# Performance work log

Measured on AMD Instinct MI355X. Metric: run time of the kernel, lower is better.

The kernel has to match this reference:

```python
import jax, jax.numpy as jnp
import numpy as np

# fbank band edges (hp.bandmode == 'fbank'), 32 bands over 257 freq bins
EBAND = [0,3,5,8,10,13,15,18,22,25,29,33,38,42,48,53,59,66,73,80,89,97,107,117,128,140,153,167,183,199,216,256]

def _inverse_filter():
    f = np.zeros((len(EBAND), EBAND[-1] + 1), np.float32)
    for i in range(len(EBAND) - 1):
        w = EBAND[i + 1] - EBAND[i]
        for j in range(w):
            f[i, EBAND[i] + j] = 1.0 - j / w
            f[i + 1, EBAND[i] + j] = j / w
    return jnp.asarray(f)  # [32, 257]

def _glin(x, w):
    # GroupedLinear (DeepFilterNet-style, no bias): w [g, in/g, out/g]
    g, gi, go = w.shape
    y = jnp.einsum('...gi,gio->...go', x.reshape(x.shape[:-1] + (g, gi)), w)
    return y.reshape(x.shape[:-1] + (g * go,))

def _prelu(x, a):
    return jnp.where(x >= 0, x, a * x)

def _gru(x, wih, whh, bih, bhh):
    # single-layer torch-style GRU; x [T,B,I], wih/whh [3H, I/H]
    H = whh.shape[-1]
    h0 = jnp.zeros((x.shape[1], H), x.dtype)
    def step(h, xt):
        gi = xt @ wih.T + bih
        gh = h @ whh.T + bhh
        ir, iz, inn = jnp.split(gi, 3, axis=-1)
        hr, hz, hn = jnp.split(gh, 3, axis=-1)
        r = jax.nn.sigmoid(ir + hr)
        z = jax.nn.sigmoid(iz + hz)
        n = jnp.tanh(inn + r * hn)
        hnew = (1.0 - z) * n + z * h
        return hnew, hnew
    _, ys = jax.lax.scan(step, h0, x)
    return ys  # [T,B,H]

def _ggru_layer(x, wih, whh, bih, bhh):
    # grouped GRU layer: weights stacked on leading group axis
    g = wih.shape[0]
    T, B, I = x.shape
    xg = x.reshape(T, B, g, I // g).transpose(2, 0, 1, 3)  # [g,T,B,I/g]
    ys = jax.vmap(_gru)(xg, wih, whh, bih, bhh)            # [g,T,B,H/g]
    return ys.transpose(1, 2, 0, 3).reshape(T, B, -1)

def _shuffle(x, g):
    # channel shuffle between grouped GRU layers
    T, B, H = x.shape
    return x.reshape(T, B, -1, g).swapaxes(2, 3).reshape(T, B, H)

def _forward(main_input, spec, log_power_input, s1_fc_in_w, s1_fc_in_b,
             s1_gru_wih0, s1_gru_whh0, s1_gru_bih0, s1_gru_bhh0,
             s1_gru_wih1, s1_gru_whh1, s1_gru_bih1, s1_gru_bhh1,
             s1_fcout_w, fc_in_low_w, prelu_low, fc_in_high_w, prelu_high,
             gru_low_wih, gru_low_whh, gru_low_bih, gru_low_bhh,
             gru_high_wih, gru_high_whh, gru_high_bih, gru_high_bhh,
             fc_out_low_w, fc_out_high_w, ne, fc):
    B, _, T, F = main_input.shape
    # --- Stage1: pad time, unfold window, keep first ne+1 taps ---
    xp = jnp.pad(main_input, ((0, 0), (0, 0), (ne, ne), (0, 0)))
    win = jnp.stack([xp[:, :, k:k + T] for k in range(ne + 1)], axis=-1)  # [B,1,T,F,ne+1]
    x = win.reshape(B, T, F * (ne + 1))                                   # [B,T,64]
    x0 = (x @ s1_fc_in_w.T + s1_fc_in_b).transpose(1, 0, 2)               # [T,B,32]
    y1 = _gru(x0, s1_gru_wih0, s1_gru_whh0, s1_gru_bih0, s1_gru_bhh0)
    y2 = _gru(y1, s1_gru_wih1, s1_gru_whh1, s1_gru_bih1, s1_gru_bhh1)
    x1 = (y1 + y2).transpose(1, 0, 2)                                     # add_outputs; [B,T,32]
    band_mask = jax.nn.sigmoid(_glin(x1, s1_fcout_w))                     # [B,T,32]
    full_mask = (band_mask @ _inverse_filter()).transpose(0, 2, 1)        # [B,257,T]
    out = spec * full_mask[..., None]                                     # [B,257,T,2]
    # --- low band path ---
    low = jnp.concatenate([log_power_input[:, :, :fc], band_mask], axis=-1)  # [B,T,160]
    low = _prelu(_glin(low, fc_in_low_w), prelu_low).transpose(1, 0, 2)      # [T,B,64]
    acc = jnp.zeros_like(low)
    inp = low
    for l in range(2):  # 2 grouped layers, shuffle between, add_outputs
        inp = _ggru_layer(inp, gru_low_wih[l], gru_low_whh[l], gru_low_bih[l], gru_low_bhh[l])
        if l == 0:
            inp = _shuffle(inp, 2)
        acc = acc + inp
    mask_low = jax.nn.sigmoid(_glin(acc.transpose(1, 0, 2), fc_out_low_w))   # [B,T,128]
    # --- high band path ---
    high = jnp.concatenate([log_power_input[:, :, fc:256], band_mask], axis=-1)  # [B,T,160]
    high = _prelu(_glin(high, fc_in_high_w), prelu_high).transpose(1, 0, 2)      # [T,B,32]
    dfh = _ggru_layer(high, gru_high_wih, gru_high_whh, gru_high_bih, gru_high_bhh)
    mask_high = jax.nn.sigmoid(_glin(dfh.transpose(1, 0, 2), fc_out_high_w))     # [B,T,128]
    # --- fuse masks (rows: 0:fc low, fc:256 high, 256 passthrough) ---
    mask = jnp.concatenate([
        mask_low.transpose(0, 2, 1) * full_mask[:, :fc],
        mask_high.transpose(0, 2, 1) * full_mask[:, fc:256],
        full_mask[:, 256:257],
    ], axis=1)                                                            # [B,257,T]
    spec_out = mask[..., None] * out
    spec_mag = jnp.sqrt(spec_out[..., 0] ** 2 + spec_out[..., 1] ** 2)
    return full_mask, mask, spec_mag, spec_out

def setup_inputs():
    ks = iter(jax.random.split(jax.random.key(0), 48))
    rn = lambda shape, s=1.0: jax.random.normal(next(ks), shape, jnp.float32) * s
    B, T = 256, 256
    return {
        'main_input': rn((B, 1, T, 32)),
        'spec': rn((B, 257, T, 2)),
        'log_power_input': rn((B, T, 256)),
        'n_expand_fbank': 1,
        'freq_cut': 128,
        's1_fc_in_w': rn((32, 64), 0.125),
        's1_fc_in_b': rn((32,), 0.05),
        's1_gru_wih0': rn((96, 32), 0.18),
        's1_gru_whh0': rn((96, 32), 0.18),
        's1_gru_bih0': rn((96,), 0.05),
        's1_gru_bhh0': rn((96,), 0.05),
        's1_gru_wih1': rn((96, 32), 0.18),
        's1_gru_whh1': rn((96, 32), 0.18),
        's1_gru_bih1': rn((96,), 0.05),
        's1_gru_bhh1': rn((96,), 0.05),
        's1_fcout_w': rn((1, 32, 32), 0.18),
        'fc_in_low_w': rn((1, 160, 64), 0.08),
        'prelu_low': jnp.full((1,), 0.25, jnp.float32),
        'fc_in_high_w': rn((2, 80, 16), 0.11),
        'prelu_high': jnp.full((1,), 0.25, jnp.float32),
        'gru_low_wih': rn((2, 2, 96, 32), 0.18),
        'gru_low_whh': rn((2, 2, 96, 32), 0.18),
        'gru_low_bih': rn((2, 2, 96), 0.05),
        'gru_low_bhh': rn((2, 2, 96), 0.05),
        'gru_high_wih': rn((2, 48, 16), 0.25),
        'gru_high_whh': rn((2, 48, 16), 0.25),
        'gru_high_bih': rn((2, 48), 0.05),
        'gru_high_bhh': rn((2, 48), 0.05),
        'fc_out_low_w': rn((1, 64, 128), 0.125),
        'fc_out_high_w': rn((2, 16, 64), 0.25),
    }

def reference(main_input, spec, log_power_input, n_expand_fbank, freq_cut,
              s1_fc_in_w, s1_fc_in_b,
              s1_gru_wih0, s1_gru_whh0, s1_gru_bih0, s1_gru_bhh0,
              s1_gru_wih1, s1_gru_whh1, s1_gru_bih1, s1_gru_bhh1,
              s1_fcout_w, fc_in_low_w, prelu_low, fc_in_high_w, prelu_high,
              gru_low_wih, gru_low_whh, gru_low_bih, gru_low_bhh,
              gru_high_wih, gru_high_whh, gru_high_bih, gru_high_bhh,
              fc_out_low_w, fc_out_high_w):
    return _forward(main_input, spec, log_power_input, s1_fc_in_w, s1_fc_in_b,
                    s1_gru_wih0, s1_gru_whh0, s1_gru_bih0, s1_gru_bhh0,
                    s1_gru_wih1, s1_gru_whh1, s1_gru_bih1, s1_gru_bhh1,
                    s1_fcout_w, fc_in_low_w, prelu_low, fc_in_high_w, prelu_high,
                    gru_low_wih, gru_low_whh, gru_low_bih, gru_low_bhh,
                    gru_high_wih, gru_high_whh, gru_high_bih, gru_high_bhh,
                    fc_out_low_w, fc_out_high_w, int(n_expand_fbank), int(freq_cut))
```

## Files before the change

### kernel.cpp

```cpp
#include <hip/hip_runtime.h>
#include <math.h>

#define Bn 256
#define Tn 256

__constant__ int EB[32] = {0,3,5,8,10,13,15,18,22,25,29,33,38,42,48,53,59,66,73,80,89,97,107,117,128,140,153,167,183,199,216,256};

__device__ __forceinline__ float fsig(float x){ return __builtin_amdgcn_rcpf(1.f + __expf(-x)); }
__device__ __forceinline__ float ftanh(float x){ return 1.f - 2.f*__builtin_amdgcn_rcpf(1.f + __expf(2.f*x)); }

__device__ __forceinline__ void gload16(const float* g, float* l){
  __builtin_amdgcn_global_load_lds((const __attribute__((address_space(1))) void*)g,
                                   (__attribute__((address_space(3))) void*)l, 16, 0, 0);
}

#define KEEP(x) asm volatile("" : "+v"(x))

typedef float v2f __attribute__((ext_vector_type(2)));

#define DOT16(res, X, W) do{ float _s0=0.f,_s1=0.f,_s2=0.f,_s3=0.f; \
  _Pragma("unroll") for (int _e=0;_e<4;++_e){ \
    _s0=fmaf((X)[_e],(W)[_e],_s0); _s1=fmaf((X)[4+_e],(W)[4+_e],_s1); \
    _s2=fmaf((X)[8+_e],(W)[8+_e],_s2); _s3=fmaf((X)[12+_e],(W)[12+_e],_s3);} \
  (res)=(_s0+_s1)+(_s2+_s3); }while(0)

#define DOT8(res, X, W) do{ float _s0=0.f,_s1=0.f; \
  _Pragma("unroll") for (int _e=0;_e<4;++_e){ \
    _s0=fmaf((X)[_e],(W)[_e],_s0); _s1=fmaf((X)[4+_e],(W)[4+_e],_s1);} \
  (res)=_s0+_s1; }while(0)

#define FMA44(A, X, W) do{ \
  (A)[0]=fmaf((X).x,(W)[0].x,(A)[0]); (A)[1]=fmaf((X).x,(W)[0].y,(A)[1]); (A)[2]=fmaf((X).x,(W)[0].z,(A)[2]); (A)[3]=fmaf((X).x,(W)[0].w,(A)[3]); \
  (A)[0]=fmaf((X).y,(W)[1].x,(A)[0]); (A)[1]=fmaf((X).y,(W)[1].y,(A)[1]); (A)[2]=fmaf((X).y,(W)[1].z,(A)[2]); (A)[3]=fmaf((X).y,(W)[1].w,(A)[3]); \
  (A)[0]=fmaf((X).z,(W)[2].x,(A)[0]); (A)[1]=fmaf((X).z,(W)[2].y,(A)[1]); (A)[2]=fmaf((X).z,(W)[2].z,(A)[2]); (A)[3]=fmaf((X).z,(W)[2].w,(A)[3]); \
  (A)[0]=fmaf((X).w,(W)[3].x,(A)[0]); (A)[1]=fmaf((X).w,(W)[3].y,(A)[1]); (A)[2]=fmaf((X).w,(W)[3].z,(A)[2]); (A)[3]=fmaf((X).w,(W)[3].w,(A)[3]); \
}while(0)

__global__ __launch_bounds__(256) void k0(const float* __restrict__ wfc, const float* __restrict__ bfc,
    const float* __restrict__ wih0, const float* __restrict__ bih0,
    const float* __restrict__ glw_ih, const float* __restrict__ glb_ih,
    const float* __restrict__ ghw_ih, const float* __restrict__ ghb_ih,
    float* __restrict__ wcT, float* __restrict__ bc,
    float* __restrict__ wBT, float* __restrict__ bB){
  int i = blockIdx.x*256 + threadIdx.x;
  if (i < 6144){
    int k = i/96, o = i - (i/96)*96;
    float s = 0.f;
    #pragma unroll
    for (int kk = 0; kk < 32; ++kk) s = fmaf(wih0[o*32+kk], wfc[kk*64+k], s);
    wcT[i] = s;
  } else if (i < 6240){
    int o = i - 6144;
    float s = bih0[o];
    #pragma unroll
    for (int kk = 0; kk < 32; ++kk) s = fmaf(wih0[o*32+kk], bfc[kk], s);
    bc[o] = s;
  } else if (i < 13920){
    int j = i - 6240;
    if (j < 6144){
      int og = j >> 7, rem = j & 127, k = rem >> 2, jj = rem & 3;
      int o = og*4 + jj; int g = o/96, r = o - g*96;
      wBT[j] = glw_ih[(g*96 + r)*32 + k];
    } else {
      int j2 = j - 6144;
      int oh = j2 >> 6, rem = j2 & 63, k = rem >> 2, jj = rem & 3;
      int o = oh*4 + jj; int g = o/48, r = o - g*48;
      wBT[j] = ghw_ih[(g*48 + r)*16 + k];
    }
  } else if (i < 14208){
// ... 21 lines not shown
  const int og = tid >> 3, btg = tid & 7;
  if (og >= 24) return;
  float acc[4][4];
  #pragma unroll
  for (int bj = 0; bj < 4; ++bj){ acc[bj][0]=0.f; acc[bj][1]=0.f; acc[bj][2]=0.f; acc[bj][3]=0.f; }
  for (int fq = 0; fq < 8; ++fq){
    float4 wvp[4], wvc[4];
    #pragma unroll
    for (int i = 0; i < 4; ++i){
      int f = fq*4 + i;
      wvp[i] = *(const float4*)&wcT[(2*f)*96 + og*4];
      wvc[i] = *(const float4*)&wcT[(2*f+1)*96 + og*4];
    }
    #pragma unroll
    for (int bj = 0; bj < 4; ++bj){
      int btl = btg + 8*bj;
      float4 xp = *(const float4*)&mbuf[btl*36 + fq*4];
      float4 xc = *(const float4*)&mbuf[(btl+1)*36 + fq*4];
      FMA44(acc[bj], xp, wvp);
      FMA44(acc[bj], xc, wvc);
    }
  }
  float4 bias = *(const float4*)&bc[og*4];
  #pragma unroll
  for (int bj = 0; bj < 4; ++bj){
    int btl = btg + 8*bj;
    float4 o;
    o.x = acc[bj][0] + bias.x; o.y = acc[bj][1] + bias.y;
    o.z = acc[bj][2] + bias.z; o.w = acc[bj][3] + bias.w;
    *(float4*)&gi0[(bt0 + btl)*96 + og*4] = o;
  }
}

__global__ __launch_bounds__(128,1) void kS1(const float* __restrict__ gi0,
    const float* __restrict__ whh0, const float* __restrict__ bhh0,
    const float* __restrict__ wih1, const float* __restrict__ whh1,
    const float* __restrict__ bih1, const float* __restrict__ bhh1,
    const float* __restrict__ fco, float* __restrict__ bmA)
{
  __shared__ __attribute__((aligned(16))) float gib[2][3072];
  __shared__ __attribute__((aligned(16))) float y1buf[2][32];
  __shared__ __attribute__((aligned(16))) float h1arr[32];
  __shared__ __attribute__((aligned(16))) float h2arr[32];
  const int tid = threadIdx.x;
  const int wid = tid >> 6;
  const int lane = tid & 63;
  const int q = lane >> 5, h = lane & 31, ko = q*16;
  const int b = blockIdx.x;
  const float* gsrc = gi0 + b*24576;

  float wI[3][16], wH[3][16], wF[16];
  float b0, b1, b2, b3;
  if (wid == 0){
    #pragma unroll
    for (int g = 0; g < 3; ++g){
      const float* w = whh0 + (g*32+h)*32 + ko;
      #pragma unroll
      for (int k = 0; k < 16; ++k){ wI[g][k] = w[k]; wH[g][k] = w[k]; }
    }
    #pragma unroll
    for (int k = 0; k < 16; ++k) wF[k] = 0.f;
    b0 = bhh0[h]; b1 = bhh0[32+h]; b2 = bhh0[64+h]; b3 = 0.f;
    #pragma unroll
    for (int c0 = 0; c0 < 2; ++c0)
      for (int it = 0; it < 12; ++it)
        gload16(gsrc + c0*3072 + it*256 + lane*4, &gib[c0][it*256]);
    asm volatile("s_waitcnt vmcnt(0)" ::: "memory");
  } else {
    #pragma unroll
    for (int g = 0; g < 3; ++g){
      const float* wi = wih1 + (g*32+h)*32 + ko;
      const float* wh = whh1 + (g*32+h)*32 + ko;
      #pragma unroll
      for (int k = 0; k < 16; ++k){ wI[g][k] = wi[k]; wH[g][k] = wh[k]; }
    }
    #pragma unroll
    for (int k = 0; k < 16; ++k) wF[k] = fco[(ko+k)*32 + h];
    b0 = bih1[h] + bhh1[h];
    b1 = bih1[32+h] + bhh1[32+h];
    b2 = bih1[64+h];
    b3 = bhh1[64+h];
  }
  #pragma unroll
  for (int g = 0; g < 3; ++g){
    #pragma unroll
    for (int k = 0; k < 16; ++k){ KEEP(wI[g][k]); KEEP(wH[g][k]); }
  }
  #pragma unroll
  for (int k = 0; k < 16; ++k) KEEP(wF[k]);
  __syncthreads();

  float hv[16];
  #pragma unroll
  for (int k = 0; k < 16; ++k) hv[k] = 0.f;
  float hOwn = 0.f;
  float c_r = 0.f, c_z = 0.f, c_n = 0.f, p_r = 0.f, p_z = 0.f, p_n = 0.f;

  for (int s = 0; s <= Tn; ++s){
    __syncthreads();
    if (wid == 0){
      if (s < Tn){
        const int t = s;
        if ((t & 31) == 0){
          if (t){
            int c = t >> 5;
            if (c < 7){
              for (int it = 0; it < 12; ++it)
                gload16(gsrc + (c+1)*3072 + it*256 + lane*4, &gib[(c+1)&1][it*256]);
            }
          }
          const float* gt = &gib[(t>>5)&1][(t&31)*96];
          c_r = gt[h]; c_z = gt[32+h]; c_n = gt[64+h];
        } else { c_r = p_r; c_z = p_z; c_n = p_n; }
        if ((t+1) & 31){
          const float* gn = &gib[((t+1)>>5)&1][((t+1)&31)*96];
          p_r = gn[h]; p_z = gn[32+h]; p_n = gn[64+h];
        }
        float pr, pz, pn;
        DOT16(pr, hv, wI[0]); DOT16(pz, hv, wI[1]); DOT16(pn, hv, wI[2]);
        pr += __shfl_xor(pr,32); pz += __shfl_xor(pz,32); pn += __shfl_xor(pn,32);
        float r = fsig(c_r + pr + b0);
        float z = fsig(c_z + pz + b1);
        float nn = ftanh(c_n + r*(pn + b2));
        float hn = nn + z*(hOwn - nn);
        hOwn = hn;
        h1arr[h] = hn;
        if (q == 0) y1buf[s & 1][h] = hn;
        *(float4*)&hv[0]  = *(const float4*)&h1arr[ko+0];
        *(float4*)&hv[4]  = *(const float4*)&h1arr[ko+4];
        *(float4*)&hv[8]  = *(const float4*)&h1arr[ko+8];
        *(float4*)&hv[12] = *(const float4*)&h1arr[ko+12];
      }
    } else {
      if (s >= 1){
        const int t = s - 1;
        const float* yb = y1buf[t & 1];
        float xv[16];
        *(float4*)&xv[0]  = *(const float4*)&yb[ko+0];
        *(float4*)&xv[4]  = *(const float4*)&yb[ko+4];
        *(float4*)&xv[8]  = *(const float4*)&yb[ko+8];
        *(float4*)&xv[12] = *(const float4*)&yb[ko+12];
        float ur, uz, ui, vr, vz, vh;
        DOT16(ur, xv, wI[0]); DOT16(uz, xv, wI[1]); DOT16(ui, xv, wI[2]);
        DOT16(vr, hv, wH[0]); DOT16(vz, hv, wH[1]); DOT16(vh, hv, wH[2]);
        float qr = ur + vr, qz = uz + vz;
        qr += __shfl_xor(qr,32); qz += __shfl_xor(qz,32);
        ui += __shfl_xor(ui,32); vh += __shfl_xor(vh,32);
        float r1 = fsig(qr + b0);
        float z1 = fsig(qz + b1);
        float n1 = ftanh(ui + b2 + r1*(vh + b3));
        float hn = n1 + z1*(hOwn - n1);
        hOwn = hn;
        h2arr[h] = hn;
        *(float4*)&hv[0]  = *(const float4*)&h2arr[ko+0];
        *(float4*)&hv[4]  = *(const float4*)&h2arr[ko+4];
        *(float4*)&hv[8]  = *(const float4*)&h2arr[ko+8];
        *(float4*)&hv[12] = *(const float4*)&h2arr[ko+12];
        float sf = 0.f;
        #pragma unroll
        for (int k = 0; k < 16; ++k) sf = fmaf(xv[k] + hv[k], wF[k], sf);
        sf += __shfl_xor(sf,32);
        if (q == 0) bmA[(b*Tn + t)*32 + h] = fsig(sf);
      }
    }
  }
}

__global__ __launch_bounds__(256) void kP(const float* __restrict__ lpi,
    const float* __restrict__ bmA,
    const float* __restrict__ wlo, const float* __restrict__ plo,
    const float* __restrict__ whi, const float* __restrict__ phi,
    const float* __restrict__ wBT, const float* __restrict__ bB,
    float* __restrict__ giL, float* __restrict__ giH)
{
  __shared__ float xb[32*292];
  __shared__ float mb[32*100];
  const int tid = threadIdx.x;
  const int b = blockIdx.x >> 3;
  const int t0 = (blockIdx.x & 7)*32;
  const int bt0 = b*256 + t0;
  #pragma unroll
  for (int j = 0; j < 8; ++j){
    int idx = j*256 + tid;
    int row = idx >> 6, c4 = idx & 63;
    float4 v = *(const float4*)&lpi[(bt0 + row)*256 + c4*4];
    *(float4*)&xb[row*292 + c4*4] = v;
  }
  {
    int row = tid >> 3, c4 = tid & 7;
    float4 v = *(const float4*)&bmA[(bt0 + row)*32 + c4*4];
    *(float4*)&xb[row*292 + 256 + c4*4] = v;
  }
  __syncthreads();
  const int og = tid >> 3, btg = tid & 7;
  if (og < 16){
    float acc[4][4];
    #pragma unroll
    for (int bj = 0; bj < 4; ++bj){ acc[bj][0]=0.f; acc[bj][1]=0.f; acc[bj][2]=0.f; acc[bj][3]=0.f; }
    for (int kq = 0; kq < 40; ++kq){
      int k0_ = kq*4;
      int kk = (k0_ < 128) ? k0_ : k0_ + 128;
      float4 wv[4];
      #pragma unroll
      for (int i = 0; i < 4; ++i) wv[i] = *(const float4*)&wlo[(k0_+i)*64 + og*4];
      #pragma unroll
      for (int bj = 0; bj < 4; ++bj){
        float4 xv = *(const float4*)&xb[(btg + 8*bj)*292 + kk];
        FMA44(acc[bj], xv, wv);
      }
    }
    const float a = plo[0];
    #pragma unroll
    for (int bj = 0; bj < 4; ++bj){
      float4 m;
      m.x = acc[bj][0] >= 0.f ? acc[bj][0] : a*acc[bj][0];
      m.y = acc[bj][1] >= 0.f ? acc[bj][1] : a*acc[bj][1];
      m.z = acc[bj][2] >= 0.f ? acc[bj][2] : a*acc[bj][2];
      m.w = acc[bj][3] >= 0.f ? acc[bj][3] : a*acc[bj][3];
      *(float4*)&mb[(btg + 8*bj)*100 + og*4] = m;
    }
  } else if (og < 24){
    int o0 = (og - 16)*4;
    int g = o0 >> 4, r0 = o0 & 15;
    int xoff = 128 + g*80;
    float acc[4][4];
    #pragma unroll
    for (int bj = 0; bj < 4; ++bj){ acc[bj][0]=0.f; acc[bj][1]=0.f; acc[bj][2]=0.f; acc[bj][3]=0.f; }
    for (int kq = 0; kq < 20; ++kq){
      int k0_ = kq*4;
      float4 wv[4];
      #pragma unroll
      for (int i = 0; i < 4; ++i) wv[i] = *(const float4*)&whi[(g*80 + k0_ + i)*16 + r0];
      #pragma unroll
      for (int bj = 0; bj < 4; ++bj){
        float4 xv = *(const float4*)&xb[(btg + 8*bj)*292 + xoff + k0_];
        FMA44(acc[bj], xv, wv);
      }
    }
    const float a = phi[0];
    #pragma unroll
    for (int bj = 0; bj < 4; ++bj){
      float4 m;
      m.x = acc[bj][0] >= 0.f ? acc[bj][0] : a*acc[bj][0];
      m.y = acc[bj][1] >= 0.f ? acc[bj][1] : a*acc[bj][1];
      m.z = acc[bj][2] >= 0.f ? acc[bj][2] : a*acc[bj][2];
      m.w = acc[bj][3] >= 0.f ? acc[bj][3] : a*acc[bj][3];
      *(float4*)&mb[(btg + 8*bj)*100 + 64 + o0] = m;
    }
  }
  __syncthreads();
  for (int og2 = og; og2 < 72; og2 += 32){
    int woff, kbase, K, obase, dstride;
    float* dst;
    float4 bias;
    if (og2 < 48){
      woff = og2*128; kbase = (og2 >= 24) ? 32 : 0; K = 32;
      obase = og2*4; dst = giL; dstride = 192;
      bias = *(const float4*)&bB[obase];
    } else {
      int oh = og2 - 48;
      woff = 6144 + oh*64;
      int o0 = oh*4; int g = o0/48;
      kbase = 64 + g*16; K = 16;
      obase = o0; dst = giH; dstride = 96;
      bias = *(const float4*)&bB[192 + o0];
    }
    float acc[4][4];
    #pragma unroll
    for (int bj = 0; bj < 4; ++bj){ acc[bj][0]=0.f; acc[bj][1]=0.f; acc[bj][2]=0.f; acc[bj][3]=0.f; }
// ... 195 lines not shown
            asm volatile("s_waitcnt vmcnt(6)" ::: "memory");
          } else {
            asm volatile("s_waitcnt vmcnt(0)" ::: "memory");
          }
        }
        const float* gt = &gib[((t>>4)&1)*1536 + (t&15)*96 + g*48];
        c_r = gt[h]; c_z = gt[16+h]; c_n = gt[32+h];
      } else { c_r = p_r; c_z = p_z; c_n = p_n; }
      if ((t+1) & 15){
        const float* gn = &gib[(((t+1)>>4)&1)*1536 + ((t+1)&15)*96 + g*48];
        p_r = gn[h]; p_z = gn[16+h]; p_n = gn[32+h];
      }
      float pr, pz, pn;
      DOT8(pr, hv, ah[0]); DOT8(pz, hv, ah[1]); DOT8(pn, hv, ah[2]);
      pr += __shfl_xor(pr,16); pz += __shfl_xor(pz,16); pn += __shfl_xor(pn,16);
      float r = fsig(c_r + pr + bhr);
      float z = fsig(c_z + pz + bhz);
      float nn = ftanh(c_n + r*(pn + bhn));
      float hn = nn + z*(hOwn - nn);
      hOwn = hn;
      harr[g*16 + h] = hn;
      *(float4*)&hv[0] = *(const float4*)&harr[g*16 + ko + 0];
      *(float4*)&hv[4] = *(const float4*)&harr[g*16 + ko + 4];
      if (qh == 0) dfh[(b*256 + t)*32 + g*16 + h] = hn;
    }
  }
}

__global__ __launch_bounds__(256) void k7(const float* __restrict__ acc,
    const float* __restrict__ dfh, const float* __restrict__ bmA,
    const float* __restrict__ wlo, const float* __restrict__ whi,
    const float* __restrict__ spec, float* __restrict__ out)
{
  __shared__ float accs[32][65];
  __shared__ float dfhs[32][33];
  __shared__ float bmt[32][33];
  __shared__ float frcs[257];
  __shared__ int   ibds[257];
  const int tid = threadIdx.x;
  const int b  = blockIdx.x >> 3;
  const int t0 = (blockIdx.x & 7) * 32;
  for (int idx = tid; idx < 32*16; idx += 256){
    int tl = idx >> 4, c4 = (idx & 15)*4;
    float4 v = *(const float4*)&acc[(b*256 + t0 + tl)*64 + c4];
    accs[tl][c4] = v.x; accs[tl][c4+1] = v.y; accs[tl][c4+2] = v.z; accs[tl][c4+3] = v.w;
  }
  for (int idx = tid; idx < 32*8; idx += 256){
    int tl = idx >> 3, c4 = (idx & 7)*4;
    float4 v = *(const float4*)&dfh[(b*256 + t0 + tl)*32 + c4];
    dfhs[tl][c4] = v.x; dfhs[tl][c4+1] = v.y; dfhs[tl][c4+2] = v.z; dfhs[tl][c4+3] = v.w;
    float4 u = *(const float4*)&bmA[(b*Tn + t0 + tl)*32 + c4];
    bmt[tl][c4] = u.x; bmt[tl][c4+1] = u.y; bmt[tl][c4+2] = u.z; bmt[tl][c4+3] = u.w;
  }
  for (int f = tid; f < 257; f += 256){
    int i = 0;
    #pragma unroll
    for (int k = 1; k < 31; ++k) if (f >= EB[k]) i = k;
    ibds[f] = i;
    frcs[f] = (f < 256) ? (float)(f - EB[i]) / (float)(EB[i+1] - EB[i]) : 0.f;
  }
  __syncthreads();
  const int tl = tid & 31, fo = tid >> 5;
  float* out1 = out + 16842752;
  float* out2 = out + 2*16842752;
  float* out3 = out + 3*16842752;
  const float2* sp2 = (const float2*)spec;
  {
    float p[16];
    #pragma unroll
    for (int j = 0; j < 16; ++j) p[j] = 0.f;
    for (int i = 0; i < 64; ++i){
      float a = accs[tl][i];
      const float4* wr = (const float4*)&wlo[i*128 + fo*16];
      #pragma unroll
      for (int j4 = 0; j4 < 4; ++j4){
        float4 wv = wr[j4];
        p[j4*4+0] = fmaf(a, wv.x, p[j4*4+0]);
        p[j4*4+1] = fmaf(a, wv.y, p[j4*4+1]);
        p[j4*4+2] = fmaf(a, wv.z, p[j4*4+2]);
        p[j4*4+3] = fmaf(a, wv.w, p[j4*4+3]);
      }
    }
    #pragma unroll
    for (int j = 0; j < 16; ++j){
      int f = fo*16 + j;
      int i = ibds[f]; float fr = frcs[f];
      float full = bmt[tl][i]*(1.f - fr) + bmt[tl][i+1]*fr;
      float m = fsig(p[j])*full;
      int base = (b*257 + f)*Tn + t0 + tl;
      float2 s = sp2[base];
      float fm = full*m;
      float sx = s.x*fm, sy = s.y*fm;
      out[base]  = full;
      out1[base] = m;
      out2[base] = sqrtf(sx*sx + sy*sy);
      *(v2f*)&out3[base*2] = (v2f){sx, sy};
    }
  }
  {
    float p[16];
    #pragma unroll
    for (int j = 0; j < 16; ++j) p[j] = 0.f;
    const int g = fo >> 2, ob = (fo & 3)*16;
    for (int i = 0; i < 16; ++i){
      float a = dfhs[tl][g*16 + i];
      const float4* wr = (const float4*)&whi[(g*16 + i)*64 + ob];
      #pragma unroll
      for (int j4 = 0; j4 < 4; ++j4){
        float4 wv = wr[j4];
        p[j4*4+0] = fmaf(a, wv.x, p[j4*4+0]);
        p[j4*4+1] = fmaf(a, wv.y, p[j4*4+1]);
        p[j4*4+2] = fmaf(a, wv.z, p[j4*4+2]);
        p[j4*4+3] = fmaf(a, wv.w, p[j4*4+3]);
      }
    }
    #pragma unroll
    for (int j = 0; j < 16; ++j){
      int f = 128 + fo*16 + j;
      int i = ibds[f]; float fr = frcs[f];
      float full = bmt[tl][i]*(1.f - fr) + bmt[tl][i+1]*fr;
      float m = fsig(p[j])*full;
      int base = (b*257 + f)*Tn + t0 + tl;
      float2 s = sp2[base];
      float fm = full*m;
      float sx = s.x*fm, sy = s.y*fm;
      out[base]  = full;
      out1[base] = m;
      out2[base] = sqrtf(sx*sx + sy*sy);
      *(v2f*)&out3[base*2] = (v2f){sx, sy};
    }
  }
  if (fo == 0){
    int base = (b*257 + 256)*Tn + t0 + tl;
    out[base]  = 0.f;
    out1[base] = 0.f;
    out2[base] = 0.f;
    *(v2f*)&out3[base*2] = (v2f){0.f, 0.f};
  }
}

extern "C" void kernel_launch(void* const* d_in, const int* in_sizes, int n_in,
                              void* d_out, int out_size, void* d_ws, size_t ws_size,
                              hipStream_t stream){
  const float* mi   = (const float*)d_in[0];
  const float* spec = (const float*)d_in[1];
  const float* lpi  = (const float*)d_in[2];
  const float* s1w  = (const float*)d_in[5];
  const float* s1b  = (const float*)d_in[6];
  const float* wih0 = (const float*)d_in[7];
  const float* whh0 = (const float*)d_in[8];
  const float* bih0 = (const float*)d_in[9];
  const float* bhh0 = (const float*)d_in[10];
  const float* wih1 = (const float*)d_in[11];
  const float* whh1 = (const float*)d_in[12];
  const float* bih1 = (const float*)d_in[13];
  const float* bhh1 = (const float*)d_in[14];
  const float* fco  = (const float*)d_in[15];
  const float* filw = (const float*)d_in[16];
  const float* plo  = (const float*)d_in[17];
  const float* fihw = (const float*)d_in[18];
  const float* phi  = (const float*)d_in[19];
  const float* glw_ih = (const float*)d_in[20];
  const float* glw_hh = (const float*)d_in[21];
  const float* glb_ih = (const float*)d_in[22];
  const float* glb_hh = (const float*)d_in[23];
  const float* ghw_ih = (const float*)d_in[24];
  const float* ghw_hh = (const float*)d_in[25];
  const float* ghb_ih = (const float*)d_in[26];
  const float* ghb_hh = (const float*)d_in[27];
  const float* folw = (const float*)d_in[28];
  const float* fohw = (const float*)d_in[29];

  float* outf = (float*)d_out;
  float* giL  = outf;
  float* gi0  = outf + 12582912;
  float* giH  = outf + 18874368;

  float* ws  = (float*)d_ws;
  float* wcT = ws;
  float* bc  = ws + 6144;
  float* wBT = ws + 6240;
  float* bB  = ws + 13920;
  float* bmA = ws + 14336;
  float* acc = ws + 2111488;
  float* dfh = ws + 6305792;
  float* out = (float*)d_out;

  k0<<<56, 256, 0, stream>>>(s1w, s1b, wih0, bih0, glw_ih, glb_ih, ghw_ih, ghb_ih,
                             wcT, bc, wBT, bB);
  k1<<<2048, 256, 0, stream>>>(mi, wcT, bc, gi0);
  kS1<<<256, 128, 0, stream>>>(gi0, whh0, bhh0, wih1, whh1, bih1, bhh1, fco, bmA);
  kP<<<2048, 256, 0, stream>>>(lpi, bmA, filw, plo, fihw, phi, wBT, bB, giL, giH);
  kR2<<<320, 256, 0, stream>>>(giL, giH, glw_ih, glw_hh, glb_ih, glb_hh,
                               ghw_hh, ghb_hh, acc, dfh);
  k7<<<2048, 256, 0, stream>>>(acc, dfh, bmA, folw, fohw, spec, out);
}
```

Before: 584.0 us.

## Overlap stage-1 GRU with log-power projection and vectorize output kernel

New measurement: 483.3 us. 17.2% less time.

```diff
diff --git a/kernel.cpp b/kernel.cpp
--- a/kernel.cpp
+++ b/kernel.cpp
@@ -15,8 +15,6 @@
 }
 
 #define KEEP(x) asm volatile("" : "+v"(x))
-
-typedef float v2f __attribute__((ext_vector_type(2)));
 
 #define DOT16(res, X, W) do{ float _s0=0.f,_s1=0.f,_s2=0.f,_s3=0.f; \
   _Pragma("unroll") for (int _e=0;_e<4;++_e){ \
@@ -35,6 +33,9 @@
   (A)[0]=fmaf((X).z,(W)[2].x,(A)[0]); (A)[1]=fmaf((X).z,(W)[2].y,(A)[1]); (A)[2]=fmaf((X).z,(W)[2].z,(A)[2]); (A)[3]=fmaf((X).z,(W)[2].w,(A)[3]); \
   (A)[0]=fmaf((X).w,(W)[3].x,(A)[0]); (A)[1]=fmaf((X).w,(W)[3].y,(A)[1]); (A)[2]=fmaf((X).w,(W)[3].z,(A)[2]); (A)[3]=fmaf((X).w,(W)[3].w,(A)[3]); \
 }while(0)
+
+#define FMA4V(P, AV, S) do{ (P).x=fmaf((AV).x,(S),(P).x); (P).y=fmaf((AV).y,(S),(P).y); \
+  (P).z=fmaf((AV).z,(S),(P).z); (P).w=fmaf((AV).w,(S),(P).w); }while(0)
 
 __global__ __launch_bounds__(256) void k0(const float* __restrict__ wfc, const float* __restrict__ bfc,
     const float* __restrict__ wih0, const float* __restrict__ bih0,
@@ -122,180 +123,240 @@
   }
 }
 
-__global__ __launch_bounds__(128,1) void kS1(const float* __restrict__ gi0,
+__global__ __launch_bounds__(128,1) void kSP(const float* __restrict__ gi0,
     const float* __restrict__ whh0, const float* __restrict__ bhh0,
     const float* __restrict__ wih1, const float* __restrict__ whh1,
     const float* __restrict__ bih1, const float* __restrict__ bhh1,
-    const float* __restrict__ fco, float* __restrict__ bmA)
+    const float* __restrict__ fco, float* __restrict__ bmA,
+    const float* __restrict__ lpi,
+    const float* __restrict__ wlo, const float* __restrict__ whi,
+    float* __restrict__ pmid)
 {
-  __shared__ __attribute__((aligned(16))) float gib[2][3072];
-  __shared__ __attribute__((aligned(16))) float y1buf[2][32];
-  __shared__ __attribute__((aligned(16))) float h1arr[32];
-  __shared__ __attribute__((aligned(16))) float h2arr[32];
+  __shared__ __attribute__((aligned(16))) float smem[8320];
   const int tid = threadIdx.x;
-  const int wid = tid >> 6;
-  const int lane = tid & 63;
-  const int q = lane >> 5, h = lane & 31, ko = q*16;
-  const int b = blockIdx.x;
-  const float* gsrc = gi0 + b*24576;
-
-  float wI[3][16], wH[3][16], wF[16];
-  float b0, b1, b2, b3;
-  if (wid == 0){
+  if (blockIdx.x < 256){
+    float* gib   = smem;
+    float* y1buf = smem + 6144;
+    float* h1arr = smem + 6208;
+    float* h2arr = smem + 6240;
+    const int wid = tid >> 6;
+    const int lane = tid & 63;
+    const int q = lane >> 5, h = lane & 31, ko = q*16;
+    const int b = blockIdx.x;
+    const float* gsrc = gi0 + b*24576;
+
+    float wI[3][16], wH[3][16], wF[16];
+    float b0, b1, b2, b3;
+    if (wid == 0){
+      #pragma unroll
+      for (int g = 0; g < 3; ++g){
+        const float* w = whh0 + (g*32+h)*32 + ko;
+        #pragma unroll
+        for (int k = 0; k < 16; ++k){ wI[g][k] = w[k]; wH[g][k] = w[k]; }
+      }
+      #pragma unroll
+      for (int k = 0; k < 16; ++k) wF[k] = 0.f;
+      b0 = bhh0[h]; b1 = bhh0[32+h]; b2 = bhh0[64+h]; b3 = 0.f;
+      #pragma unroll
+      for (int c0 = 0; c0 < 2; ++c0)
+        for (int it = 0; it < 12; ++it)
+          gload16(gsrc + c0*3072 + it*256 + lane*4, &gib[c0*3072 + it*256]);
+      asm volatile("s_waitcnt vmcnt(0)" ::: "memory");
+    } else {
+      #pragma unroll
+      for (int g = 0; g < 3; ++g){
+        const float* wi = wih1 + (g*32+h)*32 + ko;
+        const float* wh = whh1 + (g*32+h)*32 + ko;
+        #pragma unroll
+        for (int k = 0; k < 16; ++k){ wI[g][k] = wi[k]; wH[g][k] = wh[k]; }
+      }
+      #pragma unroll
+      for (int k = 0; k < 16; ++k) wF[k] = fco[(ko+k)*32 + h];
+      b0 = bih1[h] + bhh1[h];
+      b1 = bih1[32+h] + bhh1[32+h];
+      b2 = bih1[64+h];
+      b3 = bhh1[64+h];
+    }
     #pragma unroll
     for (int g = 0; g < 3; ++g){
-      const float* w = whh0 + (g*32+h)*32 + ko;
-      #pragma unroll
-      for (int k = 0; k < 16; ++k){ wI[g][k] = w[k]; wH[g][k] = w[k]; }
-    }
-    #pragma unroll
-    for (int k = 0; k < 16; ++k) wF[k] = 0.f;
-    b0 = bhh0[h]; b1 = bhh0[32+h]; b2 = bhh0[64+h]; b3 = 0.f;
-    #pragma unroll
-    for (int c0 = 0; c0 < 2; ++c0)
-      for (int it = 0; it < 12; ++it)
-        gload16(gsrc + c0*3072 + it*256 + lane*4, &gib[c0][it*256]);
-    asm volatile("s_waitcnt vmcnt(0)" ::: "memory");
+      #pragma unroll
+      for (int k = 0; k < 16; ++k){ KEEP(wI[g][k]); KEEP(wH[g][k]); }
+    }
+    #pragma unroll
+    for (int k = 0; k < 16; ++k) KEEP(wF[k]);
+    __syncthreads();
+
+    float hv[16];
+    #pragma unroll
+    for (int k = 0; k < 16; ++k) hv[k] = 0.f;
+    float hOwn = 0.f;
+    float c_r = 0.f, c_z = 0.f, c_n = 0.f, p_r = 0.f, p_z = 0.f, p_n = 0.f;
+
+    for (int s = 0; s <= Tn; ++s){
+      __syncthreads();
+      if (wid == 0){
+        if (s < Tn){
+          const int t = s;
+          if ((t & 31) == 0){
+            if (t){
+              int c = t >> 5;
+              if (c < 7){
+                for (int it = 0; it < 12; ++it)
+                  gload16(gsrc + (c+1)*3072 + it*256 + lane*4, &gib[((c+1)&1)*3072 + it*256]);
+              }
+            }
+            const float* gt = &gib[((t>>5)&1)*3072 + (t&31)*96];
+            c_r = gt[h]; c_z = gt[32+h]; c_n = gt[64+h];
+          } else { c_r = p_r; c_z = p_z; c_n = p_n; }
+          if ((t+1) & 31){
+            const float* gn = &gib[(((t+1)>>5)&1)*3072 + ((t+1)&31)*96];
+            p_r = gn[h]; p_z = gn[32+h]; p_n = gn[64+h];
+          }
+          float pr, pz, pn;
+          DOT16(pr, hv, wI[0]); DOT16(pz, hv, wI[1]); DOT16(pn, hv, wI[2]);
+          pr += __shfl_xor(pr,32); pz += __shfl_xor(pz,32); pn += __shfl_xor(pn,32);
+          float r = fsig(c_r + pr + b0);
+          float z = fsig(c_z + pz + b1);
+          float nn = ftanh(c_n + r*(pn + b2));
+          float hn = nn + z*(hOwn - nn);
+          hOwn = hn;
+          h1arr[h] = hn;
+          if (q == 0) y1buf[(s & 1)*32 + h] = hn;
+          *(float4*)&hv[0]  = *(const float4*)&h1arr[ko+0];
+          *(float4*)&hv[4]  = *(const float4*)&h1arr[ko+4];
+          *(float4*)&hv[8]  = *(const float4*)&h1arr[ko+8];
+          *(float4*)&hv[12] = *(const float4*)&h1arr[ko+12];
+        }
+      } else {
+        if (s >= 1){
+          const int t = s - 1;
+          const float* yb = &y1buf[(t & 1)*32];
+          float xv[16];
+          *(float4*)&xv[0]  = *(const float4*)&yb[ko+0];
+          *(float4*)&xv[4]  = *(const float4*)&yb[ko+4];
+          *(float4*)&xv[8]  = *(const float4*)&yb[ko+8];
+          *(float4*)&xv[12] = *(const float4*)&yb[ko+12];
+          float ur, uz, ui, vr, vz, vh;
+          DOT16(ur, xv, wI[0]); DOT16(uz, xv, wI[1]); DOT16(ui, xv, wI[2]);
+          DOT16(vr, hv, wH[0]); DOT16(vz, hv, wH[1]); DOT16(vh, hv, wH[2]);
+          float qr = ur + vr, qz = uz + vz;
+          qr += __shfl_xor(qr,32); qz += __shfl_xor(qz,32);
+          ui += __shfl_xor(ui,32); vh += __shfl_xor(vh,32);
+          float r1 = fsig(qr + b0);
+          float z1 = fsig(qz + b1);
+          float n1 = ftanh(ui + b2 + r1*(vh + b3));
+          float hn = n1 + z1*(hOwn - n1);
+          hOwn = hn;
+          h2arr[h] = hn;
+          *(float4*)&hv[0]  = *(const float4*)&h2arr[ko+0];
+          *(float4*)&hv[4]  = *(const float4*)&h2arr[ko+4];
+          *(float4*)&hv[8]  = *(const float4*)&h2arr[ko+8];
+          *(float4*)&hv[12] = *(const float4*)&h2arr[ko+12];
+          float sf = 0.f;
+          #pragma unroll
+          for (int k = 0; k < 16; ++k) sf = fmaf(xv[k] + hv[k], wF[k], sf);
+          sf += __shfl_xor(sf,32);
+          if (q == 0) bmA[(b*Tn + t)*32 + h] = fsig(sf);
+        }
+      }
+    }
   } else {
-    #pragma unroll
-    for (int g = 0; g < 3; ++g){
-      const float* wi = wih1 + (g*32+h)*32 + ko;
-      const float* wh = whh1 + (g*32+h)*32 + ko;
-      #pragma unroll
-      for (int k = 0; k < 16; ++k){ wI[g][k] = wi[k]; wH[g][k] = wh[k]; }
-    }
-    #pragma unroll
-    for (int k = 0; k < 16; ++k) wF[k] = fco[(ko+k)*32 + h];
-    b0 = bih1[h] + bhh1[h];
-    b1 = bih1[32+h] + bhh1[32+h];
-    b2 = bih1[64+h];
-    b3 = bhh1[64+h];
-  }
-  #pragma unroll
-  for (int g = 0; g < 3; ++g){
-    #pragma unroll
-    for (int k = 0; k < 16; ++k){ KEEP(wI[g][k]); KEEP(wH[g][k]); }
-  }
-  #pragma unroll
-  for (int k = 0; k < 16; ++k) KEEP(wF[k]);
-  __syncthreads();
-
-  float hv[16];
-  #pragma unroll
-  for (int k = 0; k < 16; ++k) hv[k] = 0.f;
-  float hOwn = 0.f;
-  float c_r = 0.f, c_z = 0.f, c_n = 0.f, p_r = 0.f, p_z = 0.f, p_n = 0.f;
-
-  for (int s = 0; s <= Tn; ++s){
+    float* xb = smem;
+    const int blk = blockIdx.x - 256;
+    const int b = blk >> 3;
+    const int t0 = (blk & 7)*32;
+    const int bt0 = b*256 + t0;
+    #pragma unroll
+    for (int j = 0; j < 16; ++j){
+      int idx = j*128 + tid;
+      int row = idx >> 6, c4 = idx & 63;
+      float4 v = *(const float4*)&lpi[(bt0 + row)*256 + c4*4];
+      *(float4*)&xb[row*260 + c4*4] = v;
+    }
     __syncthreads();
-    if (wid == 0){
-      if (s < Tn){
-        const int t = s;
-        if ((t & 31) == 0){
-          if (t){
-            int c = t >> 5;
-            if (c < 7){
-              for (int it = 0; it < 12; ++it)
-                gload16(gsrc + (c+1)*3072 + it*256 + lane*4, &gib[(c+1)&1][it*256]);
-            }
+    const int og = tid >> 3, btg = tid & 7;
+    for (int og2 = og; og2 < 24; og2 += 16){
+      float acc[4][4];
+      #pragma unroll
+      for (int bj = 0; bj < 4; ++bj){ acc[bj][0]=0.f; acc[bj][1]=0.f; acc[bj][2]=0.f; acc[bj][3]=0.f; }
+      int obase;
+      if (og2 < 16){
+        for (int kq = 0; kq < 32; ++kq){
+          int k0_ = kq*4;
+          float4 wv[4];
+          #pragma unroll
+          for (int i = 0; i < 4; ++i) wv[i] = *(const float4*)&wlo[(k0_+i)*64 + og2*4];
+          #pragma unroll
+          for (int bj = 0; bj < 4; ++bj){
+            float4 xv = *(const float4*)&xb[(btg + 8*bj)*260 + k0_];
+            FMA44(acc[bj], xv, wv);
           }
-          const float* gt = &gib[(t>>5)&1][(t&31)*96];
-          c_r = gt[h]; c_z = gt[32+h]; c_n = gt[64+h];
-        } else { c_r = p_r; c_z = p_z; c_n = p_n; }
-        if ((t+1) & 31){
-          const float* gn = &gib[((t+1)>>5)&1][((t+1)&31)*96];
-          p_r = gn[h]; p_z = gn[32+h]; p_n = gn[64+h];
         }
-        float pr, pz, pn;
-        DOT16(pr, hv, wI[0]); DOT16(pz, hv, wI[1]); DOT16(pn, hv, wI[2]);
-        pr += __shfl_xor(pr,32); pz += __shfl_xor(pz,32); pn += __shfl_xor(pn,32);
-        float r = fsig(c_r + pr + b0);
-        float z = fsig(c_z + pz + b1);
-        float nn = ftanh(c_n + r*(pn + b2));
-        float hn = nn + z*(hOwn - nn);
-        hOwn = hn;
-        h1arr[h] = hn;
-        if (q == 0) y1buf[s & 1][h] = hn;
-        *(float4*)&hv[0]  = *(const float4*)&h1arr[ko+0];
-        *(float4*)&hv[4]  = *(const float4*)&h1arr[ko+4];
-        *(float4*)&hv[8]  = *(const float4*)&h1arr[ko+8];
-        *(float4*)&hv[12] = *(const float4*)&h1arr[ko+12];
-      }
-    } else {
-      if (s >= 1){
-        const int t = s - 1;
-        const float* yb = y1buf[t & 1];
-        float xv[16];
-        *(float4*)&xv[0]  = *(const float4*)&yb[ko+0];
-        *(float4*)&xv[4]  = *(const float4*)&yb[ko+4];
-        *(float4*)&xv[8]  = *(const float4*)&yb[ko+8];
-        *(float4*)&xv[12] = *(const float4*)&yb[ko+12];
-        float ur, uz, ui, vr, vz, vh;
-        DOT16(ur, xv, wI[0]); DOT16(uz, xv, wI[1]); DOT16(ui, xv, wI[2]);
-        DOT16(vr, hv, wH[0]); DOT16(vz, hv, wH[1]); DOT16(vh, hv, wH[2]);
-        float qr = ur + vr, qz = uz + vz;
-        qr += __shfl_xor(qr,32); qz += __shfl_xor(qz,32);
-        ui += __shfl_xor(ui,32); vh += __shfl_xor(vh,32);
-        float r1 = fsig(qr + b0);
-        float z1 = fsig(qz + b1);
-        float n1 = ftanh(ui + b2 + r1*(vh + b3));
-        float hn = n1 + z1*(hOwn - n1);
-        hOwn = hn;
-        h2arr[h] = hn;
-        *(float4*)&hv[0]  = *(const float4*)&h2arr[ko+0];
-        *(float4*)&hv[4]  = *(const float4*)&h2arr[ko+4];
-        *(float4*)&hv[8]  = *(const float4*)&h2arr[ko+8];
-        *(float4*)&hv[12] = *(const float4*)&h2arr[ko+12];
-        float sf = 0.f;
-        #pragma unroll
-        for (int k = 0; k < 16; ++k) sf = fmaf(xv[k] + hv[k], wF[k], sf);
-        sf += __shfl_xor(sf,32);
-        if (q == 0) bmA[(b*Tn + t)*32 + h] = fsig(sf);
+        obase = og2*4;
+      } else {
+        int o0 = (og2 - 16)*4;
+        int g = o0 >> 4, r0 = o0 & 15;
+        int xoff = 128 + g*80;
+        int nk = (g == 0) ? 20 : 12;
+        for (int kq = 0; kq < nk; ++kq){
+          int k0_ = kq*4;
+          float4 wv[4];
+          #pragma unroll
+          for (int i = 0; i < 4; ++i) wv[i] = *(const float4*)&whi[(g*80 + k0_ + i)*16 + r0];
+          #pragma unroll
+          for (int bj = 0; bj < 4; ++bj){
+            float4 xv = *(const float4*)&xb[(btg + 8*bj)*260 + xoff + k0_];
+            FMA44(acc[bj], xv, wv);
+          }
+        }
+        obase = 64 + o0;
+      }
+      #pragma unroll
+      for (int bj = 0; bj < 4; ++bj){
+        int btl = btg + 8*bj;
+        float4 o;
+        o.x = acc[bj][0]; o.y = acc[bj][1]; o.z = acc[bj][2]; o.w = acc[bj][3];
+        *(float4*)&pmid[(bt0 + btl)*96 + obase] = o;
       }
     }
   }
 }
 
-__global__ __launch_bounds__(256) void kP(const float* __restrict__ lpi,
-    const float* __restrict__ bmA,
+__global__ __launch_bounds__(256) void kPb(const float* __restrict__ bmA,
+    const float* __restrict__ pmid,
     const float* __restrict__ wlo, const float* __restrict__ plo,
     const float* __restrict__ whi, const float* __restrict__ phi,
     const float* __restrict__ wBT, const float* __restrict__ bB,
     float* __restrict__ giL, float* __restrict__ giH)
 {
-  __shared__ float xb[32*292];
+  __shared__ float bmb[32*36];
   __shared__ float mb[32*100];
   const int tid = threadIdx.x;
   const int b = blockIdx.x >> 3;
   const int t0 = (blockIdx.x & 7)*32;
   const int bt0 = b*256 + t0;
-  #pragma unroll
-  for (int j = 0; j < 8; ++j){
-    int idx = j*256 + tid;
-    int row = idx >> 6, c4 = idx & 63;
-    float4 v = *(const float4*)&lpi[(bt0 + row)*256 + c4*4];
-    *(float4*)&xb[row*292 + c4*4] = v;
-  }
   {
     int row = tid >> 3, c4 = tid & 7;
     float4 v = *(const float4*)&bmA[(bt0 + row)*32 + c4*4];
-    *(float4*)&xb[row*292 + 256 + c4*4] = v;
+    *(float4*)&bmb[row*36 + c4*4] = v;
   }
   __syncthreads();
   const int og = tid >> 3, btg = tid & 7;
   if (og < 16){
     float acc[4][4];
     #pragma unroll
-    for (int bj = 0; bj < 4; ++bj){ acc[bj][0]=0.f; acc[bj][1]=0.f; acc[bj][2]=0.f; acc[bj][3]=0.f; }
-    for (int kq = 0; kq < 40; ++kq){
+    for (int bj = 0; bj < 4; ++bj){
+      float4 p = *(const float4*)&pmid[(bt0 + btg + 8*bj)*96 + og*4];
+      acc[bj][0] = p.x; acc[bj][1] = p.y; acc[bj][2] = p.z; acc[bj][3] = p.w;
+    }
+    for (int kq = 0; kq < 8; ++kq){
       int k0_ = kq*4;
-      int kk = (k0_ < 128) ? k0_ : k0_ + 128;
       float4 wv[4];
       #pragma unroll
-      for (int i = 0; i < 4; ++i) wv[i] = *(const float4*)&wlo[(k0_+i)*64 + og*4];
+      for (int i = 0; i < 4; ++i) wv[i] = *(const float4*)&wlo[(128 + k0_ + i)*64 + og*4];
       #pragma unroll
       for (int bj = 0; bj < 4; ++bj){
-        float4 xv = *(const float4*)&xb[(btg + 8*bj)*292 + kk];
+        float4 xv = *(const float4*)&bmb[(btg + 8*bj)*36 + k0_];
         FMA44(acc[bj], xv, wv);
       }
     }
@@ -312,19 +373,23 @@
   } else if (og < 24){
     int o0 = (og - 16)*4;
     int g = o0 >> 4, r0 = o0 & 15;
-    int xoff = 128 + g*80;
     float acc[4][4];
     #pragma unroll
-    for (int bj = 0; bj < 4; ++bj){ acc[bj][0]=0.f; acc[bj][1]=0.f; acc[bj][2]=0.f; acc[bj][3]=0.f; }
-    for (int kq = 0; kq < 20; ++kq){
-      int k0_ = kq*4;
-      float4 wv[4];
-      #pragma unroll
-      for (int i = 0; i < 4; ++i) wv[i] = *(const float4*)&whi[(g*80 + k0_ + i)*16 + r0];
-      #pragma unroll
-      for (int bj = 0; bj < 4; ++bj){
-        float4 xv = *(const float4*)&xb[(btg + 8*bj)*292 + xoff + k0_];
-        FMA44(acc[bj], xv, wv);
+    for (int bj = 0; bj < 4; ++bj){
+      float4 p = *(const float4*)&pmid[(bt0 + btg + 8*bj)*96 + 64 + o0];
+      acc[bj][0] = p.x; acc[bj][1] = p.y; acc[bj][2] = p.z; acc[bj][3] = p.w;
+    }
+    if (g == 1){
+      for (int kq = 0; kq < 8; ++kq){
+        int k0_ = 48 + kq*4;
+        float4 wv[4];
+        #pragma unroll
+        for (int i = 0; i < 4; ++i) wv[i] = *(const float4*)&whi[(80 + k0_ + i)*16 + r0];
+        #pragma unroll
+        for (int bj = 0; bj < 4; ++bj){
+          float4 xv = *(const float4*)&bmb[(btg + 8*bj)*36 + kq*4];
+          FMA44(acc[bj], xv, wv);
+        }
       }
     }
     const float a = phi[0];
@@ -586,25 +651,28 @@
     const float* __restrict__ wlo, const float* __restrict__ whi,
     const float* __restrict__ spec, float* __restrict__ out)
 {
-  __shared__ float accs[32][65];
-  __shared__ float dfhs[32][33];
-  __shared__ float bmt[32][33];
+  __shared__ float accsT[64*36];
+  __shared__ float dfhsT[32*36];
+  __shared__ float bmtT[32*36];
   __shared__ float frcs[257];
   __shared__ int   ibds[257];
   const int tid = threadIdx.x;
   const int b  = blockIdx.x >> 3;
   const int t0 = (blockIdx.x & 7) * 32;
-  for (int idx = tid; idx < 32*16; idx += 256){
+  for (int idx = tid; idx < 512; idx += 256){
     int tl = idx >> 4, c4 = (idx & 15)*4;
     float4 v = *(const float4*)&acc[(b*256 + t0 + tl)*64 + c4];
-    accs[tl][c4] = v.x; accs[tl][c4+1] = v.y; accs[tl][c4+2] = v.z; accs[tl][c4+3] = v.w;
-  }
-  for (int idx = tid; idx < 32*8; idx += 256){
-    int tl = idx >> 3, c4 = (idx & 7)*4;
+    accsT[(c4+0)*36 + tl] = v.x; accsT[(c4+1)*36 + tl] = v.y;
+    accsT[(c4+2)*36 + tl] = v.z; accsT[(c4+3)*36 + tl] = v.w;
+  }
+  {
+    int tl = tid >> 3, c4 = (tid & 7)*4;
     float4 v = *(const float4*)&dfh[(b*256 + t0 + tl)*32 + c4];
-    dfhs[tl][c4] = v.x; dfhs[tl][c4+1] = v.y; dfhs[tl][c4+2] = v.z; dfhs[tl][c4+3] = v.w;
+    dfhsT[(c4+0)*36 + tl] = v.x; dfhsT[(c4+1)*36 + tl] = v.y;
+    dfhsT[(c4+2)*36 + tl] = v.z; dfhsT[(c4+3)*36 + tl] = v.w;
     float4 u = *(const float4*)&bmA[(b*Tn + t0 + tl)*32 + c4];
-    bmt[tl][c4] = u.x; bmt[tl][c4+1] = u.y; bmt[tl][c4+2] = u.z; bmt[tl][c4+3] = u.w;
+    bmtT[(c4+0)*36 + tl] = u.x; bmtT[(c4+1)*36 + tl] = u.y;
+    bmtT[(c4+2)*36 + tl] = u.z; bmtT[(c4+3)*36 + tl] = u.w;
   }
   for (int f = tid; f < 257; f += 256){
     int i = 0;
@@ -614,82 +682,101 @@
     frcs[f] = (f < 256) ? (float)(f - EB[i]) / (float)(EB[i+1] - EB[i]) : 0.f;
   }
   __syncthreads();
-  const int tl = tid & 31, fo = tid >> 5;
+  const int fq = tid >> 3, tq = tid & 7;
   float* out1 = out + 16842752;
   float* out2 = out + 2*16842752;
   float* out3 = out + 3*16842752;
-  const float2* sp2 = (const float2*)spec;
+
   {
-    float p[16];
-    #pragma unroll
-    for (int j = 0; j < 16; ++j) p[j] = 0.f;
+    float4 p[4];
+    #pragma unroll
+    for (int jf = 0; jf < 4; ++jf) p[jf] = make_float4(0.f,0.f,0.f,0.f);
     for (int i = 0; i < 64; ++i){
-      float a = accs[tl][i];
-      const float4* wr = (const float4*)&wlo[i*128 + fo*16];
-      #pragma unroll
-      for (int j4 = 0; j4 < 4; ++j4){
-        float4 wv = wr[j4];
-        p[j4*4+0] = fmaf(a, wv.x, p[j4*4+0]);
-        p[j4*4+1] = fmaf(a, wv.y, p[j4*4+1]);
-        p[j4*4+2] = fmaf(a, wv.z, p[j4*4+2]);
-        p[j4*4+3] = fmaf(a, wv.w, p[j4*4+3]);
-      }
-    }
-    #pragma unroll
-    for (int j = 0; j < 16; ++j){
-      int f = fo*16 + j;
+      float4 av = *(const float4*)&accsT[i*36 + tq*4];
+      float4 wv = *(const float4*)&wlo[i*128 + fq*4];
+      FMA4V(p[0], av, wv.x); FMA4V(p[1], av, wv.y);
+      FMA4V(p[2], av, wv.z); FMA4V(p[3], av, wv.w);
+    }
+    #pragma unroll
+    for (int jf = 0; jf < 4; ++jf){
+      int f = fq*4 + jf;
       int i = ibds[f]; float fr = frcs[f];
-      float full = bmt[tl][i]*(1.f - fr) + bmt[tl][i+1]*fr;
-      float m = fsig(p[j])*full;
-      int base = (b*257 + f)*Tn + t0 + tl;
-      float2 s = sp2[base];
-      float fm = full*m;
-      float sx = s.x*fm, sy = s.y*fm;
-      out[base]  = full;
-      out1[base] = m;
-      out2[base] = sqrtf(sx*sx + sy*sy);
-      *(v2f*)&out3[base*2] = (v2f){sx, sy};
+      float4 b0v = *(const float4*)&bmtT[i*36 + tq*4];
+      float4 b1v = *(const float4*)&bmtT[(i+1)*36 + tq*4];
+      float4 full;
+      full.x = b0v.x*(1.f-fr) + b1v.x*fr; full.y = b0v.y*(1.f-fr) + b1v.y*fr;
+      full.z = b0v.z*(1.f-fr) + b1v.z*fr; full.w = b0v.w*(1.f-fr) + b1v.w*fr;
+      float4 m;
+      m.x = fsig(p[jf].x)*full.x; m.y = fsig(p[jf].y)*full.y;
+      m.z = fsig(p[jf].z)*full.z; m.w = fsig(p[jf].w)*full.w;
+      int base = (b*257 + f)*Tn + t0 + tq*4;
+      float4 s01 = *(const float4*)&spec[base*2];
+      float4 s23 = *(const float4*)&spec[base*2 + 4];
+      float fm0 = full.x*m.x, fm1 = full.y*m.y, fm2 = full.z*m.z, fm3 = full.w*m.w;
+      float sx0 = s01.x*fm0, sy0 = s01.y*fm0;
+      float sx1 = s01.z*fm1, sy1 = s01.w*fm1;
+      float sx2 = s23.x*fm2, sy2 = s23.y*fm2;
+      float sx3 = s23.z*fm3, sy3 = s23.w*fm3;
+      *(float4*)&out[base]  = full;
+      *(float4*)&out1[base] = m;
+      float4 mag;
+      mag.x = sqrtf(sx0*sx0 + sy0*sy0); mag.y = sqrtf(sx1*sx1 + sy1*sy1);
+      mag.z = sqrtf(sx2*sx2 + sy2*sy2); mag.w = sqrtf(sx3*sx3 + sy3*sy3);
+      *(float4*)&out2[base] = mag;
+      *(float4*)&out3[base*2]     = make_float4(sx0, sy0, sx1, sy1);
+      *(float4*)&out3[base*2 + 4] = make_float4(sx2, sy2, sx3, sy3);
     }
   }
   {
-    float p[16];
-    #pragma unroll
-    for (int j = 0; j < 16; ++j) p[j] = 0.f;
-    const int g = fo >> 2, ob = (fo & 3)*16;
+    const int g = fq >> 4;
+    const int col = (fq & 15)*4;
+    float4 p[4];
+    #pragma unroll
+    for (int jf = 0; jf < 4; ++jf) p[jf] = make_float4(0.f,0.f,0.f,0.f);
     for (int i = 0; i < 16; ++i){
-      float a = dfhs[tl][g*16 + i];
-      const float4* wr = (const float4*)&whi[(g*16 + i)*64 + ob];
-      #pragma unroll
-      for (int j4 = 0; j4 < 4; ++j4){
-        float4 wv = wr[j4];
-        p[j4*4+0] = fmaf(a, wv.x, p[j4*4+0]);
-        p[j4*4+1] = fmaf(a, wv.y, p[j4*4+1]);
-        p[j4*4+2] = fmaf(a, wv.z, p[j4*4+2]);
-        p[j4*4+3] = fmaf(a, wv.w, p[j4*4+3]);
-      }
-    }
-    #pragma unroll
-    for (int j = 0; j < 16; ++j){
-      int f = 128 + fo*16 + j;
+      float4 dv = *(const float4*)&dfhsT[(g*16 + i)*36 + tq*4];
+      float4 wv = *(const float4*)&whi[(g*16 + i)*64 + col];
+      FMA4V(p[0], dv, wv.x); FMA4V(p[1], dv, wv.y);
+      FMA4V(p[2], dv, wv.z); FMA4V(p[3], dv, wv.w);
+    }
+    #pragma unroll
+    for (int jf = 0; jf < 4; ++jf){
+      int f = 128 + fq*4 + jf;
       int i = ibds[f]; float fr = frcs[f];
-      float full = bmt[tl][i]*(1.f - fr) + bmt[tl][i+1]*fr;
-      float m = fsig(p[j])*full;
-      int base = (b*257 + f)*Tn + t0 + tl;
-      float2 s = sp2[base];
-      float fm = full*m;
-      float sx = s.x*fm, sy = s.y*fm;
-      out[base]  = full;
-      out1[base] = m;
-      out2[base] = sqrtf(sx*sx + sy*sy);
-      *(v2f*)&out3[base*2] = (v2f){sx, sy};
-    }
-  }
-  if (fo == 0){
-    int base = (b*257 + 256)*Tn + t0 + tl;
-    out[base]  = 0.f;
-    out1[base] = 0.f;
-    out2[base] = 0.f;
-    *(v2f*)&out3[base*2] = (v2f){0.f, 0.f};
+      float4 b0v = *(const float4*)&bmtT[i*36 + tq*4];
+      float4 b1v = *(const float4*)&bmtT[(i+1)*36 + tq*4];
+      float4 full;
+      full.x = b0v.x*(1.f-fr) + b1v.x*fr; full.y = b0v.y*(1.f-fr) + b1v.y*fr;
+      full.z = b0v.z*(1.f-fr) + b1v.z*fr; full.w = b0v.w*(1.f-fr) + b1v.w*fr;
+      float4 m;
+      m.x = fsig(p[jf].x)*full.x; m.y = fsig(p[jf].y)*full.y;
+      m.z = fsig(p[jf].z)*full.z; m.w = fsig(p[jf].w)*full.w;
+      int base = (b*257 + f)*Tn + t0 + tq*4;
+      float4 s01 = *(const float4*)&spec[base*2];
+      float4 s23 = *(const float4*)&spec[base*2 + 4];
+      float fm0 = full.x*m.x, fm1 = full.y*m.y, fm2 = full.z*m.z, fm3 = full.w*m.w;
+      float sx0 = s01.x*fm0, sy0 = s01.y*fm0;
+      float sx1 = s01.z*fm1, sy1 = s01.w*fm1;
+      float sx2 = s23.x*fm2, sy2 = s23.y*fm2;
+      float sx3 = s23.z*fm3, sy3 = s23.w*fm3;
+      *(float4*)&out[base]  = full;
+      *(float4*)&out1[base] = m;
+      float4 mag;
+      mag.x = sqrtf(sx0*sx0 + sy0*sy0); mag.y = sqrtf(sx1*sx1 + sy1*sy1);
+      mag.z = sqrtf(sx2*sx2 + sy2*sy2); mag.w = sqrtf(sx3*sx3 + sy3*sy3);
+      *(float4*)&out2[base] = mag;
+      *(float4*)&out3[base*2]     = make_float4(sx0, sy0, sx1, sy1);
+      *(float4*)&out3[base*2 + 4] = make_float4(sx2, sy2, sx3, sy3);
+    }
+  }
+  if (tid < 8){
+    int base = (b*257 + 256)*Tn + t0 + tid*4;
+    float4 z = make_float4(0.f,0.f,0.f,0.f);
+    *(float4*)&out[base]  = z;
+    *(float4*)&out1[base] = z;
+    *(float4*)&out2[base] = z;
+    *(float4*)&out3[base*2]     = z;
+    *(float4*)&out3[base*2 + 4] = z;
   }
 }
 
@@ -730,21 +817,23 @@
   float* gi0  = outf + 12582912;
   float* giH  = outf + 18874368;
 
-  float* ws  = (float*)d_ws;
-  float* wcT = ws;
-  float* bc  = ws + 6144;
-  float* wBT = ws + 6240;
-  float* bB  = ws + 13920;
-  float* bmA = ws + 14336;
-  float* acc = ws + 2111488;
-  float* dfh = ws + 6305792;
-  float* out = (float*)d_out;
+  float* ws   = (float*)d_ws;
+  float* wcT  = ws;
+  float* bc   = ws + 6144;
+  float* wBT  = ws + 6240;
+  float* bB   = ws + 13920;
+  float* bmA  = ws + 14336;
+  float* acc  = ws + 2111488;
+  float* dfh  = ws + 6305792;
+  float* pmid = ws + 8402944;
+  float* out  = (float*)d_out;
 
   k0<<<56, 256, 0, stream>>>(s1w, s1b, wih0, bih0, glw_ih, glb_ih, ghw_ih, ghb_ih,
                              wcT, bc, wBT, bB);
   k1<<<2048, 256, 0, stream>>>(mi, wcT, bc, gi0);
-  kS1<<<256, 128, 0, stream>>>(gi0, whh0, bhh0, wih1, whh1, bih1, bhh1, fco, bmA);
-  kP<<<2048, 256, 0, stream>>>(lpi, bmA, filw, plo, fihw, phi, wBT, bB, giL, giH);
+  kSP<<<2304, 128, 0, stream>>>(gi0, whh0, bhh0, wih1, whh1, bih1, bhh1, fco, bmA,
+                                lpi, filw, fihw, pmid);
+  kPb<<<2048, 256, 0, stream>>>(bmA, pmid, filw, plo, fihw, phi, wBT, bB, giL, giH);
   kR2<<<320, 256, 0, stream>>>(giL, giH, glw_ih, glw_hh, glb_ih, glb_hh,
                                ghw_hh, ghb_hh, acc, dfh);
   k7<<<2048, 256, 0, stream>>>(acc, dfh, bmA, folw, fohw, spec, out);
```
